# Kernel tuning notes

Measured on AMD Instinct MI355X. Metric: run time of the kernel, lower is better.

Reference implementation:

```python
import jax, jax.numpy as jnp
import numpy as np

UP_KERNEL = 5  # CARAFEPack default
SCALE = 2


def conv2d(x, w, b, padding=0):
    out = jax.lax.conv_general_dilated(
        x, w, window_strides=(1, 1),
        padding=[(padding, padding), (padding, padding)],
        dimension_numbers=("NCHW", "OIHW", "NCHW"))
    return out + b[None, :, None, None]


def pixel_shuffle(x, s):
    n, c, h, w = x.shape
    co = c // (s * s)
    x = x.reshape(n, co, s, s, h, w)
    x = x.transpose(0, 1, 4, 2, 5, 3)  # n, co, h, s, w, s
    return x.reshape(n, co, h * s, w * s)


def setup_inputs() -> dict:
    key = jax.random.key(0)
    ks = jax.random.split(key, 7)
    inp = {
        "x": jax.random.normal(ks[0], (8, 1, 513, 513), jnp.float32),
        "conv_w": jax.random.normal(ks[1], (1, 1, 2, 2), jnp.float32) * 0.5,
        "conv_b": jax.random.normal(ks[2], (1,), jnp.float32) * 0.1,
        "comp_w": jax.random.normal(ks[3], (64, 1, 1, 1), jnp.float32) * 0.5,
        "comp_b": jax.random.normal(ks[4], (64,), jnp.float32) * 0.1,
        "enc_w": jax.random.normal(ks[5], (100, 64, 3, 3), jnp.float32) * 0.05,
        "enc_b": jax.random.normal(ks[6], (100,), jnp.float32) * 0.1,
    }
    return inp


def reference(x, conv_w, conv_b, comp_w, comp_b, enc_w, enc_b):
    k, s = UP_KERNEL, SCALE
    # leading valid conv, kernel 2 -> [N,1,H,W] with H=W=512
    feat = conv2d(x, conv_w, conv_b, padding=0)
    n, c, h, w = feat.shape
    # CARAFEPack: compress channels, predict reassembly kernels
    comp = conv2d(feat, comp_w, comp_b, padding=0)          # [N,64,H,W]
    mask = conv2d(comp, enc_w, enc_b, padding=1)            # [N,k^2*s^2,H,W]
    mask = pixel_shuffle(mask, s)                            # [N,k^2,sH,sW]
    mask = jax.nn.softmax(mask, axis=1)                      # normalize over k^2
    # unfold feat into kxk neighborhoods (pad = (k-1)//2)
    pad = (k - 1) // 2
    xp = jnp.pad(feat, ((0, 0), (0, 0), (pad, pad), (pad, pad)))
    patches = jnp.stack(
        [xp[:, :, i:i + h, j:j + w] for i in range(k) for j in range(k)],
        axis=2)                                              # [N,C,k^2,H,W]
    # each output pixel (h*s+a, w*s+b) uses the kernel at that upsampled loc
    maskr = mask.reshape(n, k * k, h, s, w, s)
    out = jnp.einsum("nckhw,nkhawb->nchawb", patches, maskr)
    return out.reshape(n, c, h * s, w * s)
```

## Files before the change

### kernel.cpp

```cpp
#include <hip/hip_runtime.h>

typedef float v2f    __attribute__((ext_vector_type(2)));
typedef float f32x16 __attribute__((ext_vector_type(16)));
typedef __bf16 bf16x8 __attribute__((ext_vector_type(8)));

#define H 512
#define W 512
#define XH 513
#define L2E 1.4426950408889634f

#define WS_DELTA 2048

__device__ inline void row2ch(int r, int& q, int& j) {
  q = (r & 1) + 2 * ((r >> 2) & 1);
  j = ((r >> 1) & 1) + 2 * ((r >> 3) & 3) + 8 * (r >> 5);
}

__device__ inline unsigned bf16_rne(float f) {
  unsigned u = __float_as_uint(f);
  return (u + 0x7FFFu + ((u >> 16) & 1u)) >> 16;
}

__device__ inline unsigned cvtpk(float lo, float hi_) {
  unsigned r;
  asm("v_cvt_pk_bf16_f32 %0, %1, %2" : "=v"(r) : "v"(lo), "v"(hi_));
  return r;
}

__global__ __launch_bounds__(1024)
void prep_kernel(const float* comp_w, const float* comp_b,
                 const float* enc_w, const float* enc_b,
                 unsigned* ws) {
  __shared__ float sWe[900];
  __shared__ float sBc[900];
  int t = threadIdx.x;
  if (t < 900) {
    int o = t / 9, tap = t % 9;
    float sw = 0.f, sb = 0.f;
    for (int c = 0; c < 64; ++c) {
      float e = enc_w[(o * 64 + c) * 9 + tap];
      sw += e * comp_w[c];
      sb += e * comp_b[c];
    }
    sWe[t] = sw * L2E;
    sBc[t] = sb * L2E;
  }
  __syncthreads();
  if (t < 128) {
    int r = t, q, j;
    row2ch(r, q, j);
    unsigned k1[16], k2[16];
    #pragma unroll
    for (int k = 0; k < 16; ++k) { k1[k] = 0; k2[k] = 0; }
    if (j < 25) {
      int o = j * 4 + q;
      unsigned wh[9], wl[9];
      float base = enc_b[o] * L2E;
      for (int tap = 0; tap < 9; ++tap) base += sBc[o * 9 + tap];
      for (int tap = 0; tap < 9; ++tap) {
        float wf = sWe[o * 9 + tap];
        unsigned h = bf16_rne(wf);
        wh[tap] = h;
        wl[tap] = bf16_rne(wf - __uint_as_float(h << 16));
      }
      unsigned bh = bf16_rne(base);
      unsigned bl = bf16_rne(base - __uint_as_float(bh << 16));
      for (int tap = 0; tap < 9; ++tap) k1[tap] = wh[tap];
      k1[9] = bh;
      for (int tap = 0; tap < 6; ++tap) k1[10 + tap] = wh[tap];
      for (int tap = 0; tap < 3; ++tap) k2[tap] = wh[6 + tap];
      for (int tap = 0; tap < 9; ++tap) k2[3 + tap] = wl[tap];
      k2[12] = bl;
    }
    int tt = r >> 5, m = r & 31;
    for (int kh = 0; kh < 2; ++kh) {
      int lane = m + 32 * kh;
      for (int d = 0; d < 4; ++d) {
        int k = kh * 8 + d * 2;
        ws[((0 * 4 + tt) * 64 + lane) * 4 + d] = k1[k] | (k1[k + 1] << 16);
        ws[((1 * 4 + tt) * 64 + lane) * 4 + d] = k2[k] | (k2[k + 1] << 16);
      }
    }
  }
  if (t < 1024) {
    int pat = (t >> 7) + 1, r = t & 127, q, j;
    row2ch(r, q, j);
    float dv = 0.f;
    if (j < 25) {
      int o = j * 4 + q;
      int ph = pat / 3, pw_ = pat % 3;
      for (int tap = 0; tap < 9; ++tap) {
        int dr = tap / 3, dc = tap % 3;
        bool bad = (ph == 1 && dr == 0) || (ph == 2 && dr == 2) ||
                   (pw_ == 1 && dc == 0) || (pw_ == 2 && dc == 2);
        if (bad) dv -= sBc[o * 9 + tap];
      }
    }
    ((float*)ws)[WS_DELTA + t] = dv;
  }
}

__global__ __launch_bounds__(64, 3)
void carafe_kernel(const float* x, const float* conv_w, const float* conv_b,
                   const unsigned* ws, float* out) {
  __shared__ float sF[13][36];
  __shared__ float sDelta[8][128];

  int lane = threadIdx.x;
  int n = blockIdx.z;
  int w0 = blockIdx.x * 32;
  int y0 = blockIdx.y * 8;

  float w00 = conv_w[0], w01 = conv_w[1], w10 = conv_w[2], w11 = conv_w[3];
  float cb = conv_b[0];
  const float* xn = x + (size_t)n * XH * XH;

  for (int i = lane; i < 13 * 36; i += 64) {
    int r = i / 36, c = i - r * 36;
    int hh = y0 - 2 + r, ww = w0 - 2 + c;
    float v = 0.f;
    if (hh >= 0 && hh < H && ww >= 0 && ww < W) {
      const float* p = xn + (size_t)hh * XH + ww;
      v = cb + w00 * p[0] + w01 * p[1] + w10 * p[XH] + w11 * p[XH + 1];
    }
    sF[r][c] = v;
  }
  bool borderblk = (blockIdx.x == 0) | (blockIdx.x == 15) |
                   (blockIdx.y == 0) | (blockIdx.y == 63);
  if (borderblk)
    for (int i = lane; i < 1024; i += 64)
      ((float*)sDelta)[i] = ((const float*)ws)[WS_DELTA + i];

  int pc = lane & 31, hi = lane >> 5;

  int4 A1[4], A2[4];
  #pragma unroll
  for (int t = 0; t < 4; ++t) {
    A1[t] = *(const int4*)(ws + ((0 * 4 + t) * 64 + lane) * 4);
    A2[t] = *(const int4*)(ws + ((1 * 4 + t) * 64 + lane) * 4);
  }
  __syncthreads();

  int wx = w0 + pc;
  float one = 1.0f;

  float p[5][5];
  #pragma unroll
  for (int i = 0; i < 5; ++i)
    #pragma unroll
    for (int j = 0; j < 5; ++j)
      p[i][j] = sF[i][pc + j];

  const f32x16 zeroacc = {0.f};
  int pwp = (wx == 0) ? 1 : ((wx == W - 1) ? 2 : 0);

  #pragma unroll
  for (int rr = 0; rr < 8; ++rr) {
    int hpx = y0 + rr;

    float t0 = p[1][1], t1 = p[1][2], t2 = p[1][3];
    float t3 = p[2][1], t4 = p[2][2], t5 = p[2][3];
    float t6 = p[3][1], t7 = p[3][2], t8 = p[3][3];
    unsigned d01 = cvtpk(t0, t1), d23 = cvtpk(t2, t3);
    unsigned d45 = cvtpk(t4, t5), d67 = cvtpk(t6, t7);
    unsigned d8x = cvtpk(t8, one);
    float fl0 = t0 - __uint_as_float(d01 << 16);
    float fl1 = t1 - __uint_as_float(d01 & 0xFFFF0000u);
    float fl2 = t2 - __uint_as_float(d23 << 16);
    float fl3 = t3 - __uint_as_float(d23 & 0xFFFF0000u);
    float fl4 = t4 - __uint_as_float(d45 << 16);
    float fl5 = t5 - __uint_as_float(d45 & 0xFFFF0000u);
    float fl6 = t6 - __uint_as_float(d67 << 16);
    float fl7 = t7 - __uint_as_float(d67 & 0xFFFF0000u);
    float fl8 = t8 - __uint_as_float(d8x << 16);
    unsigned l01 = cvtpk(fl0, fl1), l23 = cvtpk(fl2, fl3);
    unsigned l45 = cvtpk(fl4, fl5), l67 = cvtpk(fl6, fl7);

    int4 b1, b2;
    b1.x = hi ? d8x : d01;
    b1.y = hi ? l01 : d23;
    b1.z = hi ? l23 : d45;
    b1.w = hi ? l45 : d67;
    b2.x = hi ? cvtpk(t5, t6) : l67;
    b2.y = hi ? cvtpk(t7, t8) : cvtpk(fl8, t0);
    b2.z = hi ? 0x00003F80u : cvtpk(t1, t2);
    b2.w = hi ? 0u : cvtpk(t3, t4);

    int ph = (hpx == 0) ? 1 : ((hpx == H - 1) ? 2 : 0);
    int pat = ph * 3 + pwp;
    bool anyb = __any(pat != 0);

    v2f sP0 = {0.f, 0.f}, aP0 = {0.f, 0.f};
    v2f sP1 = {0.f, 0.f}, aP1 = {0.f, 0.f};
    #pragma unroll
    for (int t = 0; t < 4; ++t) {
      f32x16 acc = __builtin_amdgcn_mfma_f32_32x32x16_bf16(
          __builtin_bit_cast(bf16x8, A1[t]), __builtin_bit_cast(bf16x8, b1),
          zeroacc, 0, 0, 0);
      acc = __builtin_amdgcn_mfma_f32_32x32x16_bf16(
          __builtin_bit_cast(bf16x8, A2[t]), __builtin_bit_cast(bf16x8, b2),
          acc, 0, 0, 0);
      if (anyb && pat != 0) {
        const float* dl = &sDelta[pat - 1][4 * hi];
        #pragma unroll
        for (int g = 0; g < 16; ++g) {
          if (t == 3 && g > 1) continue;
          acc[g] += dl[(g & 3) + 8 * (g >> 2) + 32 * t];
        }
      }
      #pragma unroll
      for (int jl = 0; jl < 8; ++jl) {
        if (t == 3 && jl > 0) continue;
        int j = 8 * t + jl;
        v2f e;
        e.x = __builtin_amdgcn_exp2f(acc[2 * jl + 0]);
        e.y = __builtin_amdgcn_exp2f(acc[2 * jl + 1]);
        float fj = p[j / 5][j % 5];
        if (t & 1) { sP1 += e; aP1 += e * fj; }
        else       { sP0 += e; aP0 += e * fj; }
      }
    }
    v2f s01 = sP0 + sP1;
    v2f a01 = aP0 + aP1;

    float2 res;
    res.x = a01.x * __builtin_amdgcn_rcpf(s01.x);
    res.y = a01.y * __builtin_amdgcn_rcpf(s01.y);
    float* prow = out + ((size_t)n * 1024 + 2 * hpx + hi) * 1024 + 2 * wx;
    *(float2*)prow = res;

    if (rr < 7) {
      #pragma unroll
      for (int i = 0; i < 4; ++i)
        #pragma unroll
        for (int j = 0; j < 5; ++j)
          p[i][j] = p[i + 1][j];
      #pragma unroll
      for (int j = 0; j < 5; ++j)
        p[4][j] = sF[rr + 5][pc + j];
    }
  }
}

extern "C" void kernel_launch(void* const* d_in, const int* in_sizes, int n_in,
                              void* d_out, int out_size, void* d_ws, size_t ws_size,
                              hipStream_t stream) {
  const float* x      = (const float*)d_in[0];
  const float* conv_w = (const float*)d_in[1];
  const float* conv_b = (const float*)d_in[2];
  const float* comp_w = (const float*)d_in[3];
  const float* comp_b = (const float*)d_in[4];
  const float* enc_w  = (const float*)d_in[5];
  const float* enc_b  = (const float*)d_in[6];
  float* out = (float*)d_out;
  unsigned* ws = (unsigned*)d_ws;

  prep_kernel<<<1, 1024, 0, stream>>>(comp_w, comp_b, enc_w, enc_b, ws);
  carafe_kernel<<<dim3(16, 64, 8), 64, 0, stream>>>(x, conv_w, conv_b, ws, out);
}
```

Before: 61.92 us.

## Stage MFMA weight operands in LDS and use two-wave 16-row blocks

```diff
diff --git a/kernel.cpp b/kernel.cpp
--- a/kernel.cpp
+++ b/kernel.cpp
@@ -100,24 +100,29 @@
   }
 }
 
-__global__ __launch_bounds__(64, 3)
-void carafe_kernel(const float* x, const float* conv_w, const float* conv_b,
-                   const unsigned* ws, float* out) {
-  __shared__ float sF[13][36];
+__global__ __launch_bounds__(128, 4)
+void carafe_kernel(const float* __restrict__ x, const float* __restrict__ conv_w,
+                   const float* __restrict__ conv_b,
+                   const unsigned* __restrict__ ws, float* __restrict__ out) {
+  __shared__ __align__(16) int4 sA[512];
+  __shared__ float sF[21][36];
   __shared__ float sDelta[8][128];
 
-  int lane = threadIdx.x;
+  int tid = threadIdx.x;
   int n = blockIdx.z;
   int w0 = blockIdx.x * 32;
-  int y0 = blockIdx.y * 8;
+  int yb = blockIdx.y * 16;
+
+  for (int i = tid; i < 512; i += 128)
+    sA[i] = ((const int4*)ws)[i];
 
   float w00 = conv_w[0], w01 = conv_w[1], w10 = conv_w[2], w11 = conv_w[3];
   float cb = conv_b[0];
   const float* xn = x + (size_t)n * XH * XH;
 
-  for (int i = lane; i < 13 * 36; i += 64) {
+  for (int i = tid; i < 21 * 36; i += 128) {
     int r = i / 36, c = i - r * 36;
-    int hh = y0 - 2 + r, ww = w0 - 2 + c;
+    int hh = yb - 2 + r, ww = w0 - 2 + c;
     float v = 0.f;
     if (hh >= 0 && hh < H && ww >= 0 && ww < W) {
       const float* p = xn + (size_t)hh * XH + ww;
@@ -126,21 +131,17 @@
     sF[r][c] = v;
   }
   bool borderblk = (blockIdx.x == 0) | (blockIdx.x == 15) |
-                   (blockIdx.y == 0) | (blockIdx.y == 63);
+                   (blockIdx.y == 0) | (blockIdx.y == 31);
   if (borderblk)
-    for (int i = lane; i < 1024; i += 64)
+    for (int i = tid; i < 1024; i += 128)
       ((float*)sDelta)[i] = ((const float*)ws)[WS_DELTA + i];
 
+  int lane = tid & 63, wid = tid >> 6;
   int pc = lane & 31, hi = lane >> 5;
-
-  int4 A1[4], A2[4];
-  #pragma unroll
-  for (int t = 0; t < 4; ++t) {
-    A1[t] = *(const int4*)(ws + ((0 * 4 + t) * 64 + lane) * 4);
-    A2[t] = *(const int4*)(ws + ((1 * 4 + t) * 64 + lane) * 4);
-  }
   __syncthreads();
 
+  unsigned abase = (unsigned)(size_t)(&sA[0]) + (unsigned)lane * 16u;
+  int y0 = yb + wid * 8;
   int wx = w0 + pc;
   float one = 1.0f;
 
@@ -149,10 +150,14 @@
   for (int i = 0; i < 5; ++i)
     #pragma unroll
     for (int j = 0; j < 5; ++j)
-      p[i][j] = sF[i][pc + j];
+      p[i][j] = sF[wid * 8 + i][pc + j];
 
   const f32x16 zeroacc = {0.f};
   int pwp = (wx == 0) ? 1 : ((wx == W - 1) ? 2 : 0);
+
+  int4 aA1, aA2, bA1, bA2;
+  asm volatile("ds_read_b128 %0, %2\n\tds_read_b128 %1, %2 offset:4096"
+               : "=v"(aA1), "=v"(aA2) : "v"(abase));
 
   #pragma unroll
   for (int rr = 0; rr < 8; ++rr) {
@@ -194,11 +199,23 @@
     v2f sP1 = {0.f, 0.f}, aP1 = {0.f, 0.f};
     #pragma unroll
     for (int t = 0; t < 4; ++t) {
+      unsigned nat = abase + (unsigned)((((t + 1) & 3)) * 1024);
+      if (t & 1) {
+        asm volatile("ds_read_b128 %0, %2\n\tds_read_b128 %1, %2 offset:4096"
+                     : "=v"(aA1), "=v"(aA2) : "v"(nat));
+      } else {
+        asm volatile("ds_read_b128 %0, %2\n\tds_read_b128 %1, %2 offset:4096"
+                     : "=v"(bA1), "=v"(bA2) : "v"(nat));
+      }
+      asm volatile("s_waitcnt lgkmcnt(2)");
+      __builtin_amdgcn_sched_barrier(0);
+      int4 ca1 = (t & 1) ? bA1 : aA1;
+      int4 ca2 = (t & 1) ? bA2 : aA2;
       f32x16 acc = __builtin_amdgcn_mfma_f32_32x32x16_bf16(
-          __builtin_bit_cast(bf16x8, A1[t]), __builtin_bit_cast(bf16x8, b1),
+          __builtin_bit_cast(bf16x8, ca1), __builtin_bit_cast(bf16x8, b1),
           zeroacc, 0, 0, 0);
       acc = __builtin_amdgcn_mfma_f32_32x32x16_bf16(
-          __builtin_bit_cast(bf16x8, A2[t]), __builtin_bit_cast(bf16x8, b2),
+          __builtin_bit_cast(bf16x8, ca2), __builtin_bit_cast(bf16x8, b2),
           acc, 0, 0, 0);
       if (anyb && pat != 0) {
         const float* dl = &sDelta[pat - 1][4 * hi];
@@ -237,7 +254,7 @@
           p[i][j] = p[i + 1][j];
       #pragma unroll
       for (int j = 0; j < 5; ++j)
-        p[4][j] = sF[rr + 5][pc + j];
+        p[4][j] = sF[wid * 8 + rr + 5][pc + j];
     }
   }
 }
@@ -256,5 +273,5 @@
   unsigned* ws = (unsigned*)d_ws;
 
   prep_kernel<<<1, 1024, 0, stream>>>(comp_w, comp_b, enc_w, enc_b, ws);
-  carafe_kernel<<<dim3(16, 64, 8), 64, 0, stream>>>(x, conv_w, conv_b, ws, out);
-}
+  carafe_kernel<<<dim3(16, 32, 8), 128, 0, stream>>>(x, conv_w, conv_b, ws, out);
+}
```

Result: slower. 79.12 us (+27.8%).
